# Performance work log

Hardware: AMD Instinct MI355X
Metric: run time of the kernel (lower is better)

The kernel has to match this reference:

```python
import jax, jax.numpy as jnp
import numpy as np
import math

FEATURE_DIM = 512
CLASS_NUM = 100000
BATCH = 512
SCALE = 30.0
MARGIN = 0.5
# easy_margin=False branch: Threshholder=-cos(margin), out_indicator=1
THRESHOLD = -math.cos(MARGIN)
OUT_INDICATOR = 1.0


def setup_inputs() -> dict:
    key = jax.random.key(0)
    k_feat, k_w, k_lab = jax.random.split(key, 3)
    feat = jax.random.normal(k_feat, (BATCH, FEATURE_DIM), dtype=jnp.float32)
    # xavier_uniform init for weights [class_num, feature_dim]
    limit = math.sqrt(6.0 / (CLASS_NUM + FEATURE_DIM))
    weights = jax.random.uniform(k_w, (CLASS_NUM, FEATURE_DIM), dtype=jnp.float32,
                                 minval=-limit, maxval=limit)
    label = jax.random.randint(k_lab, (BATCH,), 0, CLASS_NUM, dtype=jnp.int64)
    return {"feat": feat, "weights": weights, "label": label}


def reference(feat, weights, label):
    # Normalize features and weights
    norm_feat = jnp.linalg.norm(feat, axis=-1, keepdims=True)          # [B,1]
    nfeat = feat / norm_feat                                           # [B,D]
    norm_w = jnp.linalg.norm(weights, axis=-1, keepdims=True)          # [C,1]
    nw = weights / norm_w                                              # [C,D]

    cos = jnp.matmul(nfeat, nw.T)                                      # [B,C]

    avg_w_norm = jnp.mean(norm_w)
    avg_x_norm = jnp.mean(norm_feat)

    b = feat.shape[0]
    rows = jnp.arange(b)
    cos_label = cos[rows, label]                                       # [B]

    # per-sample angle stats (degrees), vectorized replacement of the python loop
    thetas = jnp.arccos(cos_label) / jnp.pi * 180.0
    avg_theta = jnp.mean(thetas)
    min_theta = jnp.min(thetas)
    max_theta = jnp.max(thetas)
    stdv_theta = jnp.sqrt(jnp.sum((thetas - avg_theta) ** 2) / (b - 1))

    # margin tables: add margin at label column if cos > threshold, else additive penalty
    in_margin = cos_label > THRESHOLD                                  # [B] bool
    margin_vals = jnp.where(in_margin, MARGIN, 0.0).astype(cos.dtype)
    ext_vals = jnp.where(in_margin, 0.0, -MARGIN * math.sin(MARGIN)).astype(cos.dtype)
    margin_tables = jnp.zeros_like(cos).at[rows, label].set(margin_vals)
    margin_tables_ext = (jnp.zeros_like(cos).at[rows, label].set(ext_vals)) * OUT_INDICATOR

    marginal_logits = SCALE * (jnp.cos(jnp.arccos(cos) + margin_tables) + margin_tables_ext)

    return (cos, marginal_logits, avg_theta, min_theta, max_theta,
            stdv_theta, avg_w_norm, avg_x_norm)
```

## Files before the change

kernel.cpp:

```cpp
#include <hip/hip_runtime.h>
#include <hip/hip_bf16.h>

#define FEATURE_DIM 512
#define CLASS_NUM   100000
#define BATCH       512
#define CPAD        100096
#define SCALE       30.0f
#define MARGIN      0.5f

typedef unsigned short u16;
typedef __attribute__((ext_vector_type(8))) short bf16x8;
typedef __attribute__((ext_vector_type(4))) float f32x4;

__device__ __forceinline__ u16 f32_to_bf16(float f) {
    unsigned int x = __builtin_bit_cast(unsigned int, f);
    unsigned int r = (x + 0x7fffu + ((x >> 16) & 1u)) >> 16;
    return (u16)r;
}

#define GLL(g, l) __builtin_amdgcn_global_load_lds( \
    (const __attribute__((address_space(1))) void*)(g), \
    (__attribute__((address_space(3))) void*)(l), 16, 0, 0)

__global__ __launch_bounds__(256) void normalize_rows(
    const float* __restrict__ src, u16* __restrict__ dst,
    float* __restrict__ partials, int R)
{
    const int tid  = threadIdx.x;
    const int wid  = tid >> 6;
    const int lane = tid & 63;
    const int row  = blockIdx.x * 4 + wid;
    __shared__ float s_norm[4];

    float norm = 0.0f;
    u16* drow = dst + (size_t)row * FEATURE_DIM;
    if (row < R) {
        const float4* p = (const float4*)(src + (size_t)row * FEATURE_DIM);
        float4 a = p[lane];
        float4 b = p[lane + 64];
        float ss = a.x*a.x + a.y*a.y + a.z*a.z + a.w*a.w
                 + b.x*b.x + b.y*b.y + b.z*b.z + b.w*b.w;
        #pragma unroll
        for (int o = 32; o > 0; o >>= 1) ss += __shfl_xor(ss, o, 64);
        norm = sqrtf(ss);
        float inv = 1.0f / norm;
        ushort4 pa, pb;
        pa.x = f32_to_bf16(a.x * inv); pa.y = f32_to_bf16(a.y * inv);
        pa.z = f32_to_bf16(a.z * inv); pa.w = f32_to_bf16(a.w * inv);
        pb.x = f32_to_bf16(b.x * inv); pb.y = f32_to_bf16(b.y * inv);
        pb.z = f32_to_bf16(b.z * inv); pb.w = f32_to_bf16(b.w * inv);
        ushort4* q = (ushort4*)drow;
        q[lane]      = pa;
        q[lane + 64] = pb;
    } else {
        ushort4 z = {0, 0, 0, 0};
        ushort4* q = (ushort4*)drow;
        q[lane]      = z;
        q[lane + 64] = z;
    }
    if (lane == 0) s_norm[wid] = norm;
    __syncthreads();
    if (tid == 0)
        partials[blockIdx.x] = s_norm[0] + s_norm[1] + s_norm[2] + s_norm[3];
}

__global__ __launch_bounds__(512, 2) void gemm_kernel(
    const u16* __restrict__ A,
    const u16* __restrict__ B,
    float* __restrict__ cosO, float* __restrict__ logO)
{
    __shared__ u16 As[256 * 32];
    __shared__ u16 Bs[128 * 32];

    const int tid  = threadIdx.x;
    const int n0   = blockIdx.x * 128;
    const int m0   = blockIdx.y * 256;
    const int wid  = tid >> 6;
    const int lane = tid & 63;
    const int wm   = (wid & 3) << 6;
    const int wn   = (wid >> 2) << 6;
    const int quad = lane >> 4;
    const int l15  = lane & 15;

    f32x4 acc[4][4];
    #pragma unroll
    for (int i = 0; i < 4; ++i)
        #pragma unroll
        for (int j = 0; j < 4; ++j)
            acc[i][j] = (f32x4){0.f, 0.f, 0.f, 0.f};

    const int srow = tid >> 2;
    const int scol = (tid & 3) * 8;
    const u16* gA0 = A + (size_t)(m0 + srow) * FEATURE_DIM + scol;
    const u16* gA1 = gA0 + 128 * FEATURE_DIM;
    const u16* gB  = B + (size_t)(n0 + srow) * FEATURE_DIM + scol;
    u16* lA0 = As + (size_t)tid * 8;
    u16* lA1 = As + (size_t)(512 + tid) * 8;
    u16* lB  = Bs + (size_t)tid * 8;

    for (int k0 = 0; k0 < FEATURE_DIM; k0 += 32) {
        GLL(gA0 + k0, lA0);
        GLL(gA1 + k0, lA1);
        GLL(gB  + k0, lB);
        __syncthreads();

        bf16x8 af[4], bfr[4];
        #pragma unroll
        for (int mi = 0; mi < 4; ++mi)
            af[mi] = *(const bf16x8*)(As + (wm + mi * 16 + l15) * 32 + quad * 8);
        #pragma unroll
        for (int ni = 0; ni < 4; ++ni)
            bfr[ni] = *(const bf16x8*)(Bs + (wn + ni * 16 + l15) * 32 + quad * 8);

        #pragma unroll
        for (int mi = 0; mi < 4; ++mi)
            #pragma unroll
            for (int ni = 0; ni < 4; ++ni)
                acc[mi][ni] = __builtin_amdgcn_mfma_f32_16x16x32_bf16(
                    af[mi], bfr[ni], acc[mi][ni], 0, 0, 0);
        __syncthreads();
    }

    #pragma unroll
    for (int ni = 0; ni < 4; ++ni) {
        int gc = n0 + wn + ni * 16 + l15;
        if (gc < CLASS_NUM) {
            #pragma unroll
            for (int mi = 0; mi < 4; ++mi) {
                int gr0 = m0 + wm + mi * 16 + quad * 4;
                f32x4 v = acc[mi][ni];
                #pragma unroll
                for (int r = 0; r < 4; ++r) {
                    size_t idx = (size_t)(gr0 + r) * CLASS_NUM + gc;
                    cosO[idx] = v[r];
                    logO[idx] = SCALE * v[r];
                }
            }
        }
    }
}

__global__ __launch_bounds__(512) void stats_kernel(
    const float* __restrict__ cosO, float* __restrict__ logO,
    const int* __restrict__ label,
    const float* __restrict__ pw, int npw,
    const float* __restrict__ px, int npx,
    float* __restrict__ scal)
{
    const int tid  = threadIdx.x;
    const int wid  = tid >> 6;
    const int lane = tid & 63;

    __shared__ float r_sum[8], r_min[8], r_max[8], r_w[8], r_x[8], r_var[8];
    __shared__ float s_avg;

    int lab = label[tid];
    lab = max(0, min(CLASS_NUM - 1, lab));
    float x = cosO[(size_t)tid * CLASS_NUM + lab];

    const float cosm = 0.8775825618903728f;
    const float sinm = 0.4794255386042030f;
    float lg;
    if (x > -cosm)
        lg = SCALE * (x * cosm - sinm * sqrtf(fmaxf(0.f, 1.f - x * x)));
    else
        lg = SCALE * (x - MARGIN * sinm);
    logO[(size_t)tid * CLASS_NUM + lab] = lg;

    float xc = fminf(1.f, fmaxf(-1.f, x));
    float theta = acosf(xc) * 57.29577951308232f;

    float sw = 0.f;
    for (int i = tid; i < npw; i += 512) sw += pw[i];
    float sx = (tid < npx) ? px[tid] : 0.f;

    float s = theta, mn = theta, mx = theta;
    #pragma unroll
    for (int o = 32; o > 0; o >>= 1) {
        s  += __shfl_xor(s, o, 64);
        mn  = fminf(mn, __shfl_xor(mn, o, 64));
        mx  = fmaxf(mx, __shfl_xor(mx, o, 64));
        sw += __shfl_xor(sw, o, 64);
        sx += __shfl_xor(sx, o, 64);
    }
    if (lane == 0) {
        r_sum[wid] = s; r_min[wid] = mn; r_max[wid] = mx;
        r_w[wid] = sw; r_x[wid] = sx;
    }
    __syncthreads();
    if (tid == 0) {
        float ts = 0.f, tmn = r_min[0], tmx = r_max[0], tw = 0.f, tx = 0.f;
        #pragma unroll
        for (int i = 0; i < 8; ++i) {
            ts += r_sum[i];
            tmn = fminf(tmn, r_min[i]);
            tmx = fmaxf(tmx, r_max[i]);
            tw += r_w[i];
            tx += r_x[i];
        }
        float avg = ts * (1.0f / BATCH);
        s_avg = avg;
        scal[0] = avg;
        scal[1] = tmn;
        scal[2] = tmx;
        scal[4] = tw * (1.0f / CLASS_NUM);
        scal[5] = tx * (1.0f / BATCH);
    }
    __syncthreads();
    float d = theta - s_avg;
    float v = d * d;
    #pragma unroll
    for (int o = 32; o > 0; o >>= 1) v += __shfl_xor(v, o, 64);
    if (lane == 0) r_var[wid] = v;
    __syncthreads();
    if (tid == 0) {
        float tv = 0.f;
        #pragma unroll
        for (int i = 0; i < 8; ++i) tv += r_var[i];
        scal[3] = sqrtf(tv / (BATCH - 1));
    }
}

extern "C" void kernel_launch(void* const* d_in, const int* in_sizes, int n_in,
                              void* d_out, int out_size, void* d_ws, size_t ws_size,
                              hipStream_t stream)
{
    const float* feat    = (const float*)d_in[0];
    const float* weights = (const float*)d_in[1];
    const int*   label   = (const int*)d_in[2];

    float* out  = (float*)d_out;
    float* cosO = out;
    float* logO = out + (size_t)BATCH * CLASS_NUM;
    float* scal = out + 2 * (size_t)BATCH * CLASS_NUM;

    const size_t nfeat_bytes = (size_t)BATCH * FEATURE_DIM * sizeof(u16);
    const size_t nw_bytes    = (size_t)CPAD * FEATURE_DIM * sizeof(u16);
    const size_t need = nfeat_bytes + nw_bytes + (128 + CPAD / 4) * sizeof(float);
    if (ws_size < need) return;

    char* ws    = (char*)d_ws;
    u16*  nfeat = (u16*)ws;
    u16*  nw    = (u16*)(ws + nfeat_bytes);
    float* px   = (float*)(ws + nfeat_bytes + nw_bytes);
    float* pw   = px + 128;

    normalize_rows<<<BATCH / 4, 256, 0, stream>>>(feat, nfeat, px, BATCH);
    normalize_rows<<<CPAD / 4, 256, 0, stream>>>(weights, nw, pw, CLASS_NUM);

    dim3 grid(CPAD / 128, BATCH / 256);
    gemm_kernel<<<grid, 512, 0, stream>>>(nfeat, nw, cosO, logO);

    stats_kernel<<<1, 512, 0, stream>>>(cosO, logO, label,
                                        pw, CPAD / 4, px, BATCH / 4, scal);
}
```

Baseline: 696.4 us.

## Fuse weight normalization into GEMM and cover full batch per block

Drops the separate weight-normalization kernel and its bf16 workspace. The GEMM now reads fp32 weights directly, converts them to bf16 in registers, accumulates the row sum of squares, and applies the inverse norm in the epilogue. Each block now covers all 512 batch rows, so each weight row is read once and the per-block weight-norm partials are written for the stats kernel. The cost is a larger accumulator (8x4 MFMA tiles per wave), more register pressure, and synchronous global weight loads that replace async LDS loads. Rounding also moves, since normalization is applied after the bf16 product rather than before.

```diff
diff --git a/kernel.cpp b/kernel.cpp
--- a/kernel.cpp
+++ b/kernel.cpp
@@ -4,7 +4,8 @@
 #define FEATURE_DIM 512
 #define CLASS_NUM   100000
 #define BATCH       512
-#define CPAD        100096
+#define NTILE       128
+#define NBLK        782
 #define SCALE       30.0f
 #define MARGIN      0.5f
 
@@ -52,11 +53,6 @@
         ushort4* q = (ushort4*)drow;
         q[lane]      = pa;
         q[lane + 64] = pb;
-    } else {
-        ushort4 z = {0, 0, 0, 0};
-        ushort4* q = (ushort4*)drow;
-        q[lane]      = z;
-        q[lane + 64] = z;
     }
     if (lane == 0) s_norm[wid] = norm;
     __syncthreads();
@@ -64,76 +60,120 @@
         partials[blockIdx.x] = s_norm[0] + s_norm[1] + s_norm[2] + s_norm[3];
 }
 
-__global__ __launch_bounds__(512, 2) void gemm_kernel(
-    const u16* __restrict__ A,
-    const u16* __restrict__ B,
-    float* __restrict__ cosO, float* __restrict__ logO)
-{
-    __shared__ u16 As[256 * 32];
+__global__ __launch_bounds__(512, 2) void gemm_fused(
+    const u16*  __restrict__ A,
+    const float* __restrict__ W,
+    float* __restrict__ cosO, float* __restrict__ logO,
+    float* __restrict__ pw)
+{
+    __shared__ u16 As[512 * 32];
     __shared__ u16 Bs[128 * 32];
+    __shared__ float s_inv[128];
+    __shared__ float s_red[8];
 
     const int tid  = threadIdx.x;
-    const int n0   = blockIdx.x * 128;
-    const int m0   = blockIdx.y * 256;
+    const int n0   = blockIdx.x * NTILE;
     const int wid  = tid >> 6;
     const int lane = tid & 63;
-    const int wm   = (wid & 3) << 6;
+    const int wm   = (wid & 3) << 7;
     const int wn   = (wid >> 2) << 6;
     const int quad = lane >> 4;
     const int l15  = lane & 15;
 
-    f32x4 acc[4][4];
-    #pragma unroll
-    for (int i = 0; i < 4; ++i)
+    f32x4 acc[8][4];
+    #pragma unroll
+    for (int i = 0; i < 8; ++i)
         #pragma unroll
         for (int j = 0; j < 4; ++j)
             acc[i][j] = (f32x4){0.f, 0.f, 0.f, 0.f};
 
     const int srow = tid >> 2;
     const int scol = (tid & 3) * 8;
-    const u16* gA0 = A + (size_t)(m0 + srow) * FEATURE_DIM + scol;
-    const u16* gA1 = gA0 + 128 * FEATURE_DIM;
-    const u16* gB  = B + (size_t)(n0 + srow) * FEATURE_DIM + scol;
-    u16* lA0 = As + (size_t)tid * 8;
-    u16* lA1 = As + (size_t)(512 + tid) * 8;
-    u16* lB  = Bs + (size_t)tid * 8;
+    const u16* gA = A + (size_t)srow * FEATURE_DIM + scol;
+    u16* lA = As + (size_t)tid * 8;
+
+    const int   brow = n0 + srow;
+    const bool  bval = brow < CLASS_NUM;
+    const float* gW  = W + (size_t)brow * FEATURE_DIM + scol;
+
+    float ssq = 0.0f;
 
     for (int k0 = 0; k0 < FEATURE_DIM; k0 += 32) {
-        GLL(gA0 + k0, lA0);
-        GLL(gA1 + k0, lA1);
-        GLL(gB  + k0, lB);
+        GLL(gA + k0,                       lA);
+        GLL(gA + k0 + 128 * FEATURE_DIM,  lA + 4096);
+        GLL(gA + k0 + 256 * FEATURE_DIM,  lA + 8192);
+        GLL(gA + k0 + 384 * FEATURE_DIM,  lA + 12288);
+
+        float4 b0 = {0.f, 0.f, 0.f, 0.f};
+        float4 b1 = {0.f, 0.f, 0.f, 0.f};
+        if (bval) {
+            const float4* p = (const float4*)(gW + k0);
+            b0 = p[0];
+            b1 = p[1];
+        }
+        ssq += b0.x*b0.x + b0.y*b0.y + b0.z*b0.z + b0.w*b0.w
+             + b1.x*b1.x + b1.y*b1.y + b1.z*b1.z + b1.w*b1.w;
+        bf16x8 bb;
+        bb[0] = (short)f32_to_bf16(b0.x); bb[1] = (short)f32_to_bf16(b0.y);
+        bb[2] = (short)f32_to_bf16(b0.z); bb[3] = (short)f32_to_bf16(b0.w);
+        bb[4] = (short)f32_to_bf16(b1.x); bb[5] = (short)f32_to_bf16(b1.y);
+        bb[6] = (short)f32_to_bf16(b1.z); bb[7] = (short)f32_to_bf16(b1.w);
+        *(bf16x8*)(Bs + (size_t)tid * 8) = bb;
+
         __syncthreads();
 
-        bf16x8 af[4], bfr[4];
-        #pragma unroll
-        for (int mi = 0; mi < 4; ++mi)
+        bf16x8 af[8], bfr[4];
+        #pragma unroll
+        for (int mi = 0; mi < 8; ++mi)
             af[mi] = *(const bf16x8*)(As + (wm + mi * 16 + l15) * 32 + quad * 8);
         #pragma unroll
         for (int ni = 0; ni < 4; ++ni)
             bfr[ni] = *(const bf16x8*)(Bs + (wn + ni * 16 + l15) * 32 + quad * 8);
 
         #pragma unroll
-        for (int mi = 0; mi < 4; ++mi)
+        for (int mi = 0; mi < 8; ++mi)
             #pragma unroll
             for (int ni = 0; ni < 4; ++ni)
                 acc[mi][ni] = __builtin_amdgcn_mfma_f32_16x16x32_bf16(
                     af[mi], bfr[ni], acc[mi][ni], 0, 0, 0);
+
         __syncthreads();
     }
 
+    ssq += __shfl_xor(ssq, 1, 64);
+    ssq += __shfl_xor(ssq, 2, 64);
+    float norm = bval ? sqrtf(ssq) : 0.0f;
+    if ((tid & 3) == 0)
+        s_inv[srow] = bval ? (1.0f / norm) : 0.0f;
+
+    float nv = ((tid & 3) == 0) ? norm : 0.0f;
+    #pragma unroll
+    for (int o = 32; o > 0; o >>= 1) nv += __shfl_xor(nv, o, 64);
+    if (lane == 0) s_red[wid] = nv;
+    __syncthreads();
+    if (tid == 0) {
+        float t = 0.f;
+        #pragma unroll
+        for (int i = 0; i < 8; ++i) t += s_red[i];
+        pw[blockIdx.x] = t;
+    }
+
     #pragma unroll
     for (int ni = 0; ni < 4; ++ni) {
-        int gc = n0 + wn + ni * 16 + l15;
+        int c  = wn + ni * 16 + l15;
+        int gc = n0 + c;
         if (gc < CLASS_NUM) {
+            float invc = s_inv[c];
             #pragma unroll
-            for (int mi = 0; mi < 4; ++mi) {
-                int gr0 = m0 + wm + mi * 16 + quad * 4;
+            for (int mi = 0; mi < 8; ++mi) {
+                int gr0 = wm + mi * 16 + quad * 4;
                 f32x4 v = acc[mi][ni];
                 #pragma unroll
                 for (int r = 0; r < 4; ++r) {
+                    float cv = v[r] * invc;
                     size_t idx = (size_t)(gr0 + r) * CLASS_NUM + gc;
-                    cosO[idx] = v[r];
-                    logO[idx] = SCALE * v[r];
+                    cosO[idx] = cv;
+                    logO[idx] = SCALE * cv;
                 }
             }
         }
@@ -235,22 +275,18 @@
     float* scal = out + 2 * (size_t)BATCH * CLASS_NUM;
 
     const size_t nfeat_bytes = (size_t)BATCH * FEATURE_DIM * sizeof(u16);
-    const size_t nw_bytes    = (size_t)CPAD * FEATURE_DIM * sizeof(u16);
-    const size_t need = nfeat_bytes + nw_bytes + (128 + CPAD / 4) * sizeof(float);
+    const size_t need = nfeat_bytes + (128 + NBLK) * sizeof(float);
     if (ws_size < need) return;
 
-    char* ws    = (char*)d_ws;
-    u16*  nfeat = (u16*)ws;
-    u16*  nw    = (u16*)(ws + nfeat_bytes);
-    float* px   = (float*)(ws + nfeat_bytes + nw_bytes);
-    float* pw   = px + 128;
+    char*  ws    = (char*)d_ws;
+    u16*   nfeat = (u16*)ws;
+    float* px    = (float*)(ws + nfeat_bytes);
+    float* pw    = px + 128;
 
     normalize_rows<<<BATCH / 4, 256, 0, stream>>>(feat, nfeat, px, BATCH);
-    normalize_rows<<<CPAD / 4, 256, 0, stream>>>(weights, nw, pw, CLASS_NUM);
-
-    dim3 grid(CPAD / 128, BATCH / 256);
-    gemm_kernel<<<grid, 512, 0, stream>>>(nfeat, nw, cosO, logO);
+
+    gemm_fused<<<NBLK, 512, 0, stream>>>(nfeat, weights, cosO, logO, pw);
 
     stats_kernel<<<1, 512, 0, stream>>>(cosO, logO, label,
-                                        pw, CPAD / 4, px, BATCH / 4, scal);
-}
+                                        pw, NBLK, px, BATCH / 4, scal);
+}
```

After: 673.7 us. 3.3% less time.
